# Performance work log

Measured on AMD Instinct MI355X. Metric: run time of the kernel, lower is better.

## Reference

```python
import jax, jax.numpy as jnp
import numpy as np

K = 4096          # num_embeddings
D = 64            # embedding_dim
BETA = 0.25       # commitment_cost
DECAY = 0.99      # EMA decay
EPS = 1e-5        # Laplace smoothing eps


def setup_inputs() -> dict:
    key = jax.random.key(0)
    k1, k2, k3 = jax.random.split(key, 3)
    inputs = jax.random.normal(k1, (32, 1024, D), dtype=jnp.float32)
    weight = jax.random.normal(k2, (K, D), dtype=jnp.float32) * (1.0 / K)
    ema_cluster_size = jnp.ones((K,), dtype=jnp.float32)
    ema_embedding_sum = jax.random.normal(k3, (K, D), dtype=jnp.float32) * (1.0 / K)
    return {
        "inputs": inputs,
        "weight": weight,
        "ema_cluster_size": ema_cluster_size,
        "ema_embedding_sum": ema_embedding_sum,
    }


def reference(inputs, weight, ema_cluster_size, ema_embedding_sum):
    input_shape = inputs.shape
    flat = inputs.reshape(-1, D)                       # (N, D)
    distances = (
        jnp.sum(flat * flat, axis=1, keepdims=True)
        + jnp.sum(weight * weight, axis=1)
        - 2.0 * (flat @ weight.T)
    )
    encoding_indices = jnp.argmin(distances, axis=1)   # (N,) int
    quantized = weight[encoding_indices].reshape(input_shape)

    # EMA codebook update (torch does this with a one-hot (N,K) matmul;
    # segment_sum is the same math without the dense intermediate)
    new_cluster_size = jax.ops.segment_sum(
        jnp.ones_like(encoding_indices, dtype=jnp.float32), encoding_indices,
        num_segments=K)
    new_embedding_sum = jax.ops.segment_sum(flat, encoding_indices,
                                            num_segments=K)
    ema_cs = DECAY * ema_cluster_size + (1.0 - DECAY) * new_cluster_size
    ema_es = DECAY * ema_embedding_sum + (1.0 - DECAY) * new_embedding_sum
    n = jnp.sum(ema_cs)
    cs_smoothed = (ema_cs + EPS) / (n + K * EPS) * n
    new_weight = ema_es / cs_smoothed[:, None]

    # Commitment loss: beta * mse(inputs, sg(quantized))
    commitment_loss = BETA * jnp.mean(
        (inputs - jax.lax.stop_gradient(quantized)) ** 2)
    # Straight-through estimator
    quantized_st = inputs + jax.lax.stop_gradient(quantized - inputs)

    return (quantized_st, commitment_loss, encoding_indices,
            new_weight, ema_cs, ema_es)
```

## Files before the change

kernel.cpp:

```cpp
#include <hip/hip_runtime.h>

#define N_VEC   32768
#define K_CODES 4096
#define D_DIM   64
#define NELEM   2097152
#define TH_APPROX 7.5e-4f

#define OUT0_OFF 0
#define OUT1_OFF 2097152
#define OUT2_OFF 2097153
#define OUT3_OFF 2129921
#define OUT4_OFF 2392065
#define OUT5_OFF 2396161

#define WS_BNORM   0
#define WS_COUNTS  16384
#define WS_CANDC   32768
#define WS_CANDS   163840
#define WS_SUMS    163840
#define WS_WBF     1212416
#define WS_LPART   1212416
#define WS_CSPART  1277952
#define WS_PMIN    1736704

typedef short  s16x8 __attribute__((ext_vector_type(8)));
typedef float  f32x4 __attribute__((ext_vector_type(4)));

__device__ __forceinline__ unsigned short bf16rne(float f) {
    unsigned u = __float_as_uint(f);
    unsigned r = u + 0x7fffu + ((u >> 16) & 1u);
    return (unsigned short)(r >> 16);
}

__device__ __forceinline__ float np_pairwise64(const float* sq) {
    float r0 = sq[0], r1 = sq[1], r2 = sq[2], r3 = sq[3];
    float r4 = sq[4], r5 = sq[5], r6 = sq[6], r7 = sq[7];
#pragma unroll
    for (int b = 8; b < 64; b += 8) {
        r0 = __fadd_rn(r0, sq[b + 0]); r1 = __fadd_rn(r1, sq[b + 1]);
        r2 = __fadd_rn(r2, sq[b + 2]); r3 = __fadd_rn(r3, sq[b + 3]);
        r4 = __fadd_rn(r4, sq[b + 4]); r5 = __fadd_rn(r5, sq[b + 5]);
        r6 = __fadd_rn(r6, sq[b + 6]); r7 = __fadd_rn(r7, sq[b + 7]);
    }
    return __fadd_rn(__fadd_rn(__fadd_rn(r0, r1), __fadd_rn(r2, r3)),
                     __fadd_rn(__fadd_rn(r4, r5), __fadd_rn(r6, r7)));
}

__global__ void k_bnorm(const float* __restrict__ w, float* __restrict__ bn) {
    int k = blockIdx.x * 256 + threadIdx.x;
    const float* wr = w + k * D_DIM;
    float sq[64];
#pragma unroll
    for (int i = 0; i < 64; ++i) { float v = wr[i]; sq[i] = __fmul_rn(v, v); }
    bn[k] = np_pairwise64(sq);
}

__global__ void k_wcvtbf(const float* __restrict__ w, short* __restrict__ wbf) {
    int gid = blockIdx.x * 256 + threadIdx.x;
    wbf[gid] = (short)bf16rne(w[gid]);
}

#define XLDS_LD 72

#define STAGE_X_BF16                                                        \
    for (int i = tid; i < 64 * 16; i += 256) {                              \
        int r = i >> 4, c4 = i & 15;                                        \
        float4 v = ((const float4*)(x + (size_t)(rbase + r) * D_DIM))[c4];  \
        ushort4 b;                                                          \
        b.x = bf16rne(v.x); b.y = bf16rne(v.y);                             \
        b.z = bf16rne(v.z); b.w = bf16rne(v.w);                             \
        *(ushort4*)&xlds[r * XLDS_LD + c4 * 4] = b;                         \
    }

#define HOIST_A_FRAGS                                                       \
    s16x8 af0[4], af1[4];                                                   \
    _Pragma("unroll")                                                       \
    for (int rt = 0; rt < 4; ++rt) {                                        \
        af0[rt] = *(const s16x8*)&xlds[(rt * 16 + arow) * XLDS_LD + agrp * 8]; \
        af1[rt] = *(const s16x8*)&xlds[(rt * 16 + arow) * XLDS_LD + 32 + agrp * 8]; \
    }

__global__ __launch_bounds__(256, 4) void k_min(
    const float* __restrict__ x, const short* __restrict__ wbf,
    const float* __restrict__ bn, float* __restrict__ pmin) {
    __shared__ short xlds[64 * XLDS_LD];
    __shared__ float wmin[4][64];

    const int tid  = threadIdx.x;
    const int lane = tid & 63;
    const int wid  = __builtin_amdgcn_readfirstlane(tid >> 6);
    const int rg   = blockIdx.x & 511;
    const int kc   = blockIdx.x >> 9;
    const int rbase = rg * 64;
    const int arow = lane & 15;
    const int agrp = lane >> 4;

    STAGE_X_BF16
    __syncthreads();
    HOIST_A_FRAGS

    const int col0 = kc * 1024 + wid * 256;

    float rm[16];
#pragma unroll
    for (int i = 0; i < 16; ++i) rm[i] = 3.4e38f;

    for (int tc = 0; tc < 16; ++tc) {
        const int mycol = col0 + tc * 16 + arow;
        s16x8 b0 = *(const s16x8*)&wbf[(size_t)mycol * D_DIM + agrp * 8];
        s16x8 b1 = *(const s16x8*)&wbf[(size_t)mycol * D_DIM + 32 + agrp * 8];
        float bnv = bn[mycol];
#pragma unroll
        for (int rt = 0; rt < 4; ++rt) {
            f32x4 c = {0.f, 0.f, 0.f, 0.f};
            c = __builtin_amdgcn_mfma_f32_16x16x32_bf16(af0[rt], b0, c, 0, 0, 0);
            c = __builtin_amdgcn_mfma_f32_16x16x32_bf16(af1[rt], b1, c, 0, 0, 0);
#pragma unroll
            for (int j = 0; j < 4; ++j) {
                float m = fmaf(-2.0f, c[j], bnv);
                rm[rt * 4 + j] = fminf(rm[rt * 4 + j], m);
            }
        }
    }

#pragma unroll
    for (int i = 0; i < 16; ++i) {
        float v = rm[i];
        v = fminf(v, __shfl_xor(v, 1));
        v = fminf(v, __shfl_xor(v, 2));
        v = fminf(v, __shfl_xor(v, 4));
        v = fminf(v, __shfl_xor(v, 8));
        rm[i] = v;
    }
    if (arow == 0) {
#pragma unroll
        for (int i = 0; i < 16; ++i)
            wmin[wid][(i >> 2) * 16 + agrp * 4 + (i & 3)] = rm[i];
    }
    __syncthreads();
    if (tid < 64) {
        float g = fminf(fminf(wmin[0][tid], wmin[1][tid]),
                        fminf(wmin[2][tid], wmin[3][tid]));
        pmin[kc * N_VEC + rbase + tid] = g;
    }
}

__global__ __launch_bounds__(256, 4) void k_collect(
    const float* __restrict__ x, const short* __restrict__ wbf,
    const float* __restrict__ bn, const float* __restrict__ pmin,
    int* __restrict__ candc, unsigned short* __restrict__ cands) {
    __shared__ short xlds[64 * XLDS_LD];
    __shared__ float gmin[64];

    const int tid  = threadIdx.x;
    const int lane = tid & 63;
    const int wid  = __builtin_amdgcn_readfirstlane(tid >> 6);
    const int rg   = blockIdx.x & 511;
    const int kc   = blockIdx.x >> 9;
    const int rbase = rg * 64;
    const int arow = lane & 15;
    const int agrp = lane >> 4;

    STAGE_X_BF16
    if (tid < 64) {
        const int n = rbase + tid;
        float g = fminf(fminf(pmin[n], pmin[N_VEC + n]),
                        fminf(pmin[2 * N_VEC + n], pmin[3 * N_VEC + n]));
        gmin[tid] = g + TH_APPROX;
    }
    __syncthreads();
    HOIST_A_FRAGS

    float gv[16];
#pragma unroll
    for (int i = 0; i < 16; ++i)
        gv[i] = gmin[(i >> 2) * 16 + agrp * 4 + (i & 3)];

    const int col0 = kc * 1024 + wid * 256;

    for (int tc = 0; tc < 16; ++tc) {
        const int mycol = col0 + tc * 16 + arow;
        s16x8 b0 = *(const s16x8*)&wbf[(size_t)mycol * D_DIM + agrp * 8];
        s16x8 b1 = *(const s16x8*)&wbf[(size_t)mycol * D_DIM + 32 + agrp * 8];
        float bnv = bn[mycol];
#pragma unroll
        for (int rt = 0; rt < 4; ++rt) {
            f32x4 c = {0.f, 0.f, 0.f, 0.f};
            c = __builtin_amdgcn_mfma_f32_16x16x32_bf16(af0[rt], b0, c, 0, 0, 0);
            c = __builtin_amdgcn_mfma_f32_16x16x32_bf16(af1[rt], b1, c, 0, 0, 0);
#pragma unroll
            for (int j = 0; j < 4; ++j) {
                float m = fmaf(-2.0f, c[j], bnv);
                if (m <= gv[rt * 4 + j]) {
                    int n = rbase + rt * 16 + agrp * 4 + j;
                    int p = atomicAdd(&candc[n], 1);
                    if (p < 16)
                        cands[(size_t)n * 16 + p] = (unsigned short)mycol;
                }
            }
        }
    }
}

__global__ __launch_bounds__(256) void k_rescore(
    const float* __restrict__ x, const float* __restrict__ w,
    const float* __restrict__ bn, const int* __restrict__ candc,
    const unsigned short* __restrict__ cands, float* __restrict__ out_idx) {
    const int n = blockIdx.x * 256 + threadIdx.x;

    float4 xv[16];
    const float4* xr = (const float4*)(x + (size_t)n * D_DIM);
#pragma unroll
    for (int i = 0; i < 16; ++i) xv[i] = xr[i];

    float A;
    {
        float sq[64];
#pragma unroll
        for (int i = 0; i < 16; ++i) {
            sq[4*i+0] = __fmul_rn(xv[i].x, xv[i].x);
            sq[4*i+1] = __fmul_rn(xv[i].y, xv[i].y);
            sq[4*i+2] = __fmul_rn(xv[i].z, xv[i].z);
            sq[4*i+3] = __fmul_rn(xv[i].w, xv[i].w);
        }
        A = np_pairwise64(sq);
    }

    const int cnt = candc[n];
    float bestd = 3.4e38f;
    int   besti = 0;

    if (cnt <= 16) {
        unsigned short cl[16];
        for (int i = 0; i < cnt; ++i) cl[i] = cands[(size_t)n * 16 + i];
        for (int i = 1; i < cnt; ++i) {
            unsigned short v = cl[i];
            int j = i - 1;
            while (j >= 0 && cl[j] > v) { cl[j + 1] = cl[j]; --j; }
            cl[j + 1] = v;
        }
        for (int i = 0; i < cnt; ++i) {
            const int c = cl[i];
            const float4* wr = (const float4*)(w + (size_t)c * D_DIM);
            float a = 0.f;
#pragma unroll
            for (int ch = 0; ch < 16; ++ch) {
                float4 u = wr[ch];
                a = __fmaf_rn(xv[ch].x, u.x, a);
                a = __fmaf_rn(xv[ch].y, u.y, a);
                a = __fmaf_rn(xv[ch].z, u.z, a);
                a = __fmaf_rn(xv[ch].w, u.w, a);
            }
            float d = __fsub_rn(__fadd_rn(A, bn[c]), __fmul_rn(2.0f, a));
            if (d < bestd) { bestd = d; besti = c; }
        }
    } else {
        for (int c = 0; c < K_CODES; ++c) {
            const float4* wr = (const float4*)(w + (size_t)c * D_DIM);
            float a = 0.f;
#pragma unroll
            for (int ch = 0; ch < 16; ++ch) {
                float4 u = wr[ch];
                a = __fmaf_rn(xv[ch].x, u.x, a);
                a = __fmaf_rn(xv[ch].y, u.y, a);
                a = __fmaf_rn(xv[ch].z, u.z, a);
                a = __fmaf_rn(xv[ch].w, u.w, a);
            }
            float d = __fsub_rn(__fadd_rn(A, bn[c]), __fmul_rn(2.0f, a));
            if (d < bestd) { bestd = d; besti = c; }
        }
    }
    out_idx[n] = (float)besti;
}

__global__ __launch_bounds__(256) void k_quant(
    const float* __restrict__ x, const float* __restrict__ w,
    const float* __restrict__ idxf, float* __restrict__ out0,
    float* __restrict__ sums, int* __restrict__ counts,
    double* __restrict__ lpart) {
    const int gid = blockIdx.x * 256 + threadIdx.x;
    const int n = gid >> 6, d = gid & 63;
    const int idx = (int)idxf[n];
    const float in = x[gid];
    const float q  = w[idx * D_DIM + d];
    out0[gid] = in + (q - in);
    const float diff = in - q;
    atomicAdd(&sums[idx * D_DIM + d], in);
    if (d == 0) atomicAdd(&counts[idx], 1);

    __shared__ double red[256];
    red[threadIdx.x] = (double)diff * (double)diff;
    __syncthreads();
    for (int s = 128; s > 0; s >>= 1) {
        if (threadIdx.x < s) red[threadIdx.x] += red[threadIdx.x + s];
        __syncthreads();
    }
    if (threadIdx.x == 0) lpart[blockIdx.x] = red[0];
}

__global__ void k_loss(const double* __restrict__ lpart, float* __restrict__ out1) {
    __shared__ double red[256];
    double s = 0.0;
    for (int i = threadIdx.x; i < 8192; i += 256) s += lpart[i];
    red[threadIdx.x] = s;
    __syncthreads();
    for (int st = 128; st > 0; st >>= 1) {
        if (threadIdx.x < st) red[threadIdx.x] += red[threadIdx.x + st];
        __syncthreads();
    }
    if (threadIdx.x == 0) out1[0] = (float)(0.25 * red[0] / (double)NELEM);
}

__global__ void k_emacs(const float* __restrict__ old_cs, const int* __restrict__ counts,
                        float* __restrict__ out4, double* __restrict__ cspart) {
    const int k = blockIdx.x * 256 + threadIdx.x;
    const float e = 0.99f * old_cs[k] + 0.01f * (float)counts[k];
    out4[k] = e;
    __shared__ double red[256];
    red[threadIdx.x] = (double)e;
    __syncthreads();
    for (int s = 128; s > 0; s >>= 1) {
        if (threadIdx.x < s) red[threadIdx.x] += red[threadIdx.x + s];
        __syncthreads();
    }
    if (threadIdx.x == 0) cspart[blockIdx.x] = red[0];
}

__global__ __launch_bounds__(256) void k_final(
    const float* __restrict__ old_es, const float* __restrict__ sums,
    const float* __restrict__ out4, const double* __restrict__ cspart,
    float* __restrict__ out3, float* __restrict__ out5) {
    double nd = 0.0;
#pragma unroll
    for (int i = 0; i < 16; ++i) nd += cspart[i];
    const float nf = (float)nd;
    const int gid = blockIdx.x * 256 + threadIdx.x;
    const int k = gid >> 6;
    const float es = 0.99f * old_es[gid] + 0.01f * sums[gid];
    out5[gid] = es;
    const float cs = out4[k];
    const float cssm = (cs + 1e-5f) / (nf + 4096.0f * 1e-5f) * nf;
    out3[gid] = es / cssm;
}

extern "C" void kernel_launch(void* const* d_in, const int* in_sizes, int n_in,
                              void* d_out, int out_size, void* d_ws, size_t ws_size,
                              hipStream_t stream) {
    const float* x      = (const float*)d_in[0];
    const float* w      = (const float*)d_in[1];
    const float* old_cs = (const float*)d_in[2];
    const float* old_es = (const float*)d_in[3];

    float* o    = (float*)d_out;
    float* out0 = o + OUT0_OFF;
    float* out1 = o + OUT1_OFF;
    float* out2 = o + OUT2_OFF;
    float* out3 = o + OUT3_OFF;
    float* out4 = o + OUT4_OFF;
    float* out5 = o + OUT5_OFF;

    char* ws = (char*)d_ws;
    float*          bnorm  = (float*)(ws + WS_BNORM);
    int*            counts = (int*)(ws + WS_COUNTS);
    int*            candc  = (int*)(ws + WS_CANDC);
    unsigned short* cands  = (unsigned short*)(ws + WS_CANDS);
    float*          sums   = (float*)(ws + WS_SUMS);
    short*          wbf    = (short*)(ws + WS_WBF);
    double*         lpart  = (double*)(ws + WS_LPART);
    double*         cspart = (double*)(ws + WS_CSPART);
    float*          pmin   = (float*)(ws + WS_PMIN);

    hipMemsetAsync(counts, 0, K_CODES * sizeof(int), stream);
    hipMemsetAsync(candc, 0, N_VEC * sizeof(int), stream);

    k_bnorm<<<K_CODES / 256, 256, 0, stream>>>(w, bnorm);
    k_wcvtbf<<<K_CODES * D_DIM / 256, 256, 0, stream>>>(w, wbf);
    k_min<<<2048, 256, 0, stream>>>(x, wbf, bnorm, pmin);
    k_collect<<<2048, 256, 0, stream>>>(x, wbf, bnorm, pmin, candc, cands);
    k_rescore<<<N_VEC / 256, 256, 0, stream>>>(x, w, bnorm, candc, cands, out2);
    hipMemsetAsync(sums, 0, K_CODES * D_DIM * sizeof(float), stream);
    k_quant<<<NELEM / 256, 256, 0, stream>>>(x, w, out2, out0, sums, counts, lpart);
    k_loss<<<1, 256, 0, stream>>>(lpart, out1);
    k_emacs<<<K_CODES / 256, 256, 0, stream>>>(old_cs, counts, out4, cspart);
    k_final<<<K_CODES * D_DIM / 256, 256, 0, stream>>>(old_es, sums, out4, cspart,
                                                       out3, out5);
}
```

Before: 166.8 us.

## Software-pipeline codebook loads in min/collect kernels, fuse codebook prep kernels

Merges the norm and bf16-conversion kernels into one vectorized prep kernel, so the codebook is read once and one launch is saved. In k_min and k_collect, each block now covers two codebook chunks instead of one, which halves the grid and reuses the staged bf16 input rows across both chunks. The tile loop is also rewritten as a double-buffered pipeline that loads the next four column groups while the MFMAs run on the current ones. This should hide global-load latency, but it raises register pressure and leaves fewer blocks for the GPU to schedule.

New measurement: 214.5 us. 1.29x slower.

```diff
diff --git a/kernel.cpp b/kernel.cpp
--- a/kernel.cpp
+++ b/kernel.cpp
@@ -25,6 +25,7 @@
 
 typedef short  s16x8 __attribute__((ext_vector_type(8)));
 typedef float  f32x4 __attribute__((ext_vector_type(4)));
+typedef unsigned short u16x8 __attribute__((ext_vector_type(8)));
 
 __device__ __forceinline__ unsigned short bf16rne(float f) {
     unsigned u = __float_as_uint(f);
@@ -46,18 +47,31 @@
                      __fadd_rn(__fadd_rn(r4, r5), __fadd_rn(r6, r7)));
 }
 
-__global__ void k_bnorm(const float* __restrict__ w, float* __restrict__ bn) {
-    int k = blockIdx.x * 256 + threadIdx.x;
-    const float* wr = w + k * D_DIM;
+__global__ void k_prep(const float* __restrict__ w, float* __restrict__ bn,
+                       short* __restrict__ wbf) {
+    const int k = blockIdx.x * 256 + threadIdx.x;
+    const float4* wr = (const float4*)(w + (size_t)k * D_DIM);
+    float4 v[16];
+#pragma unroll
+    for (int i = 0; i < 16; ++i) v[i] = wr[i];
     float sq[64];
 #pragma unroll
-    for (int i = 0; i < 64; ++i) { float v = wr[i]; sq[i] = __fmul_rn(v, v); }
+    for (int i = 0; i < 16; ++i) {
+        sq[4*i+0] = __fmul_rn(v[i].x, v[i].x);
+        sq[4*i+1] = __fmul_rn(v[i].y, v[i].y);
+        sq[4*i+2] = __fmul_rn(v[i].z, v[i].z);
+        sq[4*i+3] = __fmul_rn(v[i].w, v[i].w);
+    }
     bn[k] = np_pairwise64(sq);
-}
-
-__global__ void k_wcvtbf(const float* __restrict__ w, short* __restrict__ wbf) {
-    int gid = blockIdx.x * 256 + threadIdx.x;
-    wbf[gid] = (short)bf16rne(w[gid]);
+#pragma unroll
+    for (int i = 0; i < 8; ++i) {
+        u16x8 o;
+        o[0] = bf16rne(v[2*i].x);   o[1] = bf16rne(v[2*i].y);
+        o[2] = bf16rne(v[2*i].z);   o[3] = bf16rne(v[2*i].w);
+        o[4] = bf16rne(v[2*i+1].x); o[5] = bf16rne(v[2*i+1].y);
+        o[6] = bf16rne(v[2*i+1].z); o[7] = bf16rne(v[2*i+1].w);
+        *(u16x8*)&wbf[(size_t)k * D_DIM + i * 8] = o;
+    }
 }
 
 #define XLDS_LD 72
@@ -80,6 +94,63 @@
         af1[rt] = *(const s16x8*)&xlds[(rt * 16 + arow) * XLDS_LD + 32 + agrp * 8]; \
     }
 
+#define LOADG(b0s, b1s, bns, T0)                                            \
+    _Pragma("unroll")                                                       \
+    for (int t_ = 0; t_ < 4; ++t_) {                                        \
+        int c_ = col0 + ((T0) + t_) * 16 + arow;                            \
+        b0s[t_] = *(const s16x8*)&wbf[(size_t)c_ * D_DIM + agrp * 8];       \
+        b1s[t_] = *(const s16x8*)&wbf[(size_t)c_ * D_DIM + 32 + agrp * 8];  \
+        bns[t_] = bn[c_];                                                   \
+    }
+
+#define COMPG_MIN(b0s, b1s, bns, T0)                                        \
+    _Pragma("unroll")                                                       \
+    for (int t_ = 0; t_ < 4; ++t_) {                                        \
+        _Pragma("unroll")                                                   \
+        for (int rt = 0; rt < 4; ++rt) {                                    \
+            f32x4 c = {0.f, 0.f, 0.f, 0.f};                                 \
+            c = __builtin_amdgcn_mfma_f32_16x16x32_bf16(af0[rt], b0s[t_], c, 0, 0, 0); \
+            c = __builtin_amdgcn_mfma_f32_16x16x32_bf16(af1[rt], b1s[t_], c, 0, 0, 0); \
+            _Pragma("unroll")                                               \
+            for (int j = 0; j < 4; ++j) {                                   \
+                float m = fmaf(-2.0f, c[j], bns[t_]);                       \
+                rm[rt * 4 + j] = fminf(rm[rt * 4 + j], m);                  \
+            }                                                               \
+        }                                                                   \
+    }
+
+#define COMPG_COL(b0s, b1s, bns, T0)                                        \
+    _Pragma("unroll")                                                       \
+    for (int t_ = 0; t_ < 4; ++t_) {                                        \
+        int c_ = col0 + ((T0) + t_) * 16 + arow;                            \
+        _Pragma("unroll")                                                   \
+        for (int rt = 0; rt < 4; ++rt) {                                    \
+            f32x4 c = {0.f, 0.f, 0.f, 0.f};                                 \
+            c = __builtin_amdgcn_mfma_f32_16x16x32_bf16(af0[rt], b0s[t_], c, 0, 0, 0); \
+            c = __builtin_amdgcn_mfma_f32_16x16x32_bf16(af1[rt], b1s[t_], c, 0, 0, 0); \
+            _Pragma("unroll")                                               \
+            for (int j = 0; j < 4; ++j) {                                   \
+                float m = fmaf(-2.0f, c[j], bns[t_]);                       \
+                if (m <= gv[rt * 4 + j]) {                                  \
+                    int n_ = rbase + rt * 16 + agrp * 4 + j;                \
+                    int p_ = atomicAdd(&candc[n_], 1);                      \
+                    if (p_ < 16)                                            \
+                        cands[(size_t)n_ * 16 + p_] = (unsigned short)c_;   \
+                }                                                           \
+            }                                                               \
+        }                                                                   \
+    }
+
+#define PIPELINE(COMPG)                                                     \
+    LOADG(ub0, ub1, ubn, 0)                                                 \
+    LOADG(vb0, vb1, vbn, 4)                                                 \
+    COMPG(ub0, ub1, ubn, 0)                                                 \
+    LOADG(ub0, ub1, ubn, 8)                                                 \
+    COMPG(vb0, vb1, vbn, 4)                                                 \
+    LOADG(vb0, vb1, vbn, 12)                                                \
+    COMPG(ub0, ub1, ubn, 8)                                                 \
+    COMPG(vb0, vb1, vbn, 12)
+
 __global__ __launch_bounds__(256, 4) void k_min(
     const float* __restrict__ x, const short* __restrict__ wbf,
     const float* __restrict__ bn, float* __restrict__ pmin) {
@@ -89,8 +160,8 @@
     const int tid  = threadIdx.x;
     const int lane = tid & 63;
     const int wid  = __builtin_amdgcn_readfirstlane(tid >> 6);
-    const int rg   = blockIdx.x & 511;
-    const int kc   = blockIdx.x >> 9;
+    const int rg   = blockIdx.x >> 1;
+    const int kc0  = (blockIdx.x & 1) * 2;
     const int rbase = rg * 64;
     const int arow = lane & 15;
     const int agrp = lane >> 4;
@@ -99,49 +170,38 @@
     __syncthreads();
     HOIST_A_FRAGS
 
-    const int col0 = kc * 1024 + wid * 256;
-
-    float rm[16];
-#pragma unroll
-    for (int i = 0; i < 16; ++i) rm[i] = 3.4e38f;
-
-    for (int tc = 0; tc < 16; ++tc) {
-        const int mycol = col0 + tc * 16 + arow;
-        s16x8 b0 = *(const s16x8*)&wbf[(size_t)mycol * D_DIM + agrp * 8];
-        s16x8 b1 = *(const s16x8*)&wbf[(size_t)mycol * D_DIM + 32 + agrp * 8];
-        float bnv = bn[mycol];
-#pragma unroll
-        for (int rt = 0; rt < 4; ++rt) {
-            f32x4 c = {0.f, 0.f, 0.f, 0.f};
-            c = __builtin_amdgcn_mfma_f32_16x16x32_bf16(af0[rt], b0, c, 0, 0, 0);
-            c = __builtin_amdgcn_mfma_f32_16x16x32_bf16(af1[rt], b1, c, 0, 0, 0);
-#pragma unroll
-            for (int j = 0; j < 4; ++j) {
-                float m = fmaf(-2.0f, c[j], bnv);
-                rm[rt * 4 + j] = fminf(rm[rt * 4 + j], m);
-            }
-        }
-    }
-
-#pragma unroll
-    for (int i = 0; i < 16; ++i) {
-        float v = rm[i];
-        v = fminf(v, __shfl_xor(v, 1));
-        v = fminf(v, __shfl_xor(v, 2));
-        v = fminf(v, __shfl_xor(v, 4));
-        v = fminf(v, __shfl_xor(v, 8));
-        rm[i] = v;
-    }
-    if (arow == 0) {
-#pragma unroll
-        for (int i = 0; i < 16; ++i)
-            wmin[wid][(i >> 2) * 16 + agrp * 4 + (i & 3)] = rm[i];
-    }
-    __syncthreads();
-    if (tid < 64) {
-        float g = fminf(fminf(wmin[0][tid], wmin[1][tid]),
-                        fminf(wmin[2][tid], wmin[3][tid]));
-        pmin[kc * N_VEC + rbase + tid] = g;
+    s16x8 ub0[4], ub1[4]; float ubn[4];
+    s16x8 vb0[4], vb1[4]; float vbn[4];
+
+    for (int kc = kc0; kc < kc0 + 2; ++kc) {
+        const int col0 = kc * 1024 + wid * 256;
+        float rm[16];
+#pragma unroll
+        for (int i = 0; i < 16; ++i) rm[i] = 3.4e38f;
+
+        PIPELINE(COMPG_MIN)
+
+#pragma unroll
+        for (int i = 0; i < 16; ++i) {
+            float v = rm[i];
+            v = fminf(v, __shfl_xor(v, 1));
+            v = fminf(v, __shfl_xor(v, 2));
+            v = fminf(v, __shfl_xor(v, 4));
+            v = fminf(v, __shfl_xor(v, 8));
+            rm[i] = v;
+        }
+        if (arow == 0) {
+#pragma unroll
+            for (int i = 0; i < 16; ++i)
+                wmin[wid][(i >> 2) * 16 + agrp * 4 + (i & 3)] = rm[i];
+        }
+        __syncthreads();
+        if (tid < 64) {
+            float g = fminf(fminf(wmin[0][tid], wmin[1][tid]),
+                            fminf(wmin[2][tid], wmin[3][tid]));
+            pmin[kc * N_VEC + rbase + tid] = g;
+        }
+        __syncthreads();
     }
 }
 
@@ -155,8 +215,8 @@
     const int tid  = threadIdx.x;
     const int lane = tid & 63;
     const int wid  = __builtin_amdgcn_readfirstlane(tid >> 6);
-    const int rg   = blockIdx.x & 511;
-    const int kc   = blockIdx.x >> 9;
+    const int rg   = blockIdx.x >> 1;
+    const int kc0  = (blockIdx.x & 1) * 2;
     const int rbase = rg * 64;
     const int arow = lane & 15;
     const int agrp = lane >> 4;
@@ -176,29 +236,12 @@
     for (int i = 0; i < 16; ++i)
         gv[i] = gmin[(i >> 2) * 16 + agrp * 4 + (i & 3)];
 
-    const int col0 = kc * 1024 + wid * 256;
-
-    for (int tc = 0; tc < 16; ++tc) {
-        const int mycol = col0 + tc * 16 + arow;
-        s16x8 b0 = *(const s16x8*)&wbf[(size_t)mycol * D_DIM + agrp * 8];
-        s16x8 b1 = *(const s16x8*)&wbf[(size_t)mycol * D_DIM + 32 + agrp * 8];
-        float bnv = bn[mycol];
-#pragma unroll
-        for (int rt = 0; rt < 4; ++rt) {
-            f32x4 c = {0.f, 0.f, 0.f, 0.f};
-            c = __builtin_amdgcn_mfma_f32_16x16x32_bf16(af0[rt], b0, c, 0, 0, 0);
-            c = __builtin_amdgcn_mfma_f32_16x16x32_bf16(af1[rt], b1, c, 0, 0, 0);
-#pragma unroll
-            for (int j = 0; j < 4; ++j) {
-                float m = fmaf(-2.0f, c[j], bnv);
-                if (m <= gv[rt * 4 + j]) {
-                    int n = rbase + rt * 16 + agrp * 4 + j;
-                    int p = atomicAdd(&candc[n], 1);
-                    if (p < 16)
-                        cands[(size_t)n * 16 + p] = (unsigned short)mycol;
-                }
-            }
-        }
+    s16x8 ub0[4], ub1[4]; float ubn[4];
+    s16x8 vb0[4], vb1[4]; float vbn[4];
+
+    for (int kc = kc0; kc < kc0 + 2; ++kc) {
+        const int col0 = kc * 1024 + wid * 256;
+        PIPELINE(COMPG_COL)
     }
 }
 
@@ -373,10 +416,9 @@
     hipMemsetAsync(counts, 0, K_CODES * sizeof(int), stream);
     hipMemsetAsync(candc, 0, N_VEC * sizeof(int), stream);
 
-    k_bnorm<<<K_CODES / 256, 256, 0, stream>>>(w, bnorm);
-    k_wcvtbf<<<K_CODES * D_DIM / 256, 256, 0, stream>>>(w, wbf);
-    k_min<<<2048, 256, 0, stream>>>(x, wbf, bnorm, pmin);
-    k_collect<<<2048, 256, 0, stream>>>(x, wbf, bnorm, pmin, candc, cands);
+    k_prep<<<K_CODES / 256, 256, 0, stream>>>(w, bnorm, wbf);
+    k_min<<<1024, 256, 0, stream>>>(x, wbf, bnorm, pmin);
+    k_collect<<<1024, 256, 0, stream>>>(x, wbf, bnorm, pmin, candc, cands);
     k_rescore<<<N_VEC / 256, 256, 0, stream>>>(x, w, bnorm, candc, cands, out2);
     hipMemsetAsync(sums, 0, K_CODES * D_DIM * sizeof(float), stream);
     k_quant<<<NELEM / 256, 256, 0, stream>>>(x, w, out2, out0, sums, counts, lpart);
```
